# Performance work log

Hardware: AMD Instinct MI355X
Metric: run time of the kernel (lower is better)

Reference implementation:

```python
import jax, jax.numpy as jnp
import numpy as np


def _conv1x1(x, w, b=None):
    # x: [B, Cin, N, S], w: [Cout, Cin], 1x1 Conv2d
    y = jnp.einsum('oc,bcns->bons', w, x)
    if b is not None:
        y = y + b[None, :, None, None]
    return y


def setup_inputs() -> dict:
    key = jax.random.key(0)
    ks = jax.random.split(key, 16)
    B, Cin, N, K = 4, 128, 16384, 16
    MID, OUT, SHARE, PT = 64, 128, 8, 10
    s = 0.05
    inp = {
        'sm_feats': jax.random.normal(ks[0], (B, Cin, N, K), jnp.float32),
        'sm_ppfs': jax.random.normal(ks[1], (B, PT, N, K), jnp.float32),
        'conv0_w': jax.random.normal(ks[2], (OUT, Cin), jnp.float32) * s,
        'conv0_b': jax.random.normal(ks[3], (OUT,), jnp.float32) * s,
        'conv1_w': jax.random.normal(ks[4], (MID, OUT), jnp.float32) * s,
        'conv1_b': jax.random.normal(ks[5], (MID,), jnp.float32) * s,
        'conv2_w': jax.random.normal(ks[6], (MID, OUT), jnp.float32) * s,
        'conv2_b': jax.random.normal(ks[7], (MID,), jnp.float32) * s,
        'conv3_w': jax.random.normal(ks[8], (MID, OUT), jnp.float32) * s,
        'conv3_b': jax.random.normal(ks[9], (MID,), jnp.float32) * s,
        'convw1_w': jax.random.normal(ks[10], (MID // SHARE, MID * K), jnp.float32) * s,
        'convw2_w': jax.random.normal(ks[11], (K * MID // SHARE, MID // SHARE), jnp.float32) * s,
        'convw2_b': jax.random.normal(ks[12], (K * MID // SHARE,), jnp.float32) * s,
        'convout_w': jax.random.normal(ks[13], (OUT, MID), jnp.float32) * s,
        'convout_b': jax.random.normal(ks[14], (OUT,), jnp.float32) * s,
        'pt1_w': jax.random.normal(ks[15], (MID, PT), jnp.float32) * s,
        'pt2_w': jax.random.normal(jax.random.fold_in(key, 99), (MID, MID), jnp.float32) * s,
    }
    return inp


def reference(sm_feats, sm_ppfs, conv0_w, conv0_b, conv1_w, conv1_b, conv2_w, conv2_b,
              conv3_w, conv3_b, convw1_w, convw2_w, convw2_b, convout_w, convout_b,
              pt1_w, pt2_w):
    xn = jax.nn.relu(_conv1x1(sm_feats, conv0_w, conv0_b))  # [B, OUT, N, K]
    x = xn[..., :1]                                          # center point feature
    identity = x
    x1 = _conv1x1(x, conv1_w, conv1_b)       # [B, MID, N, 1]
    x2 = _conv1x1(xn, conv2_w, conv2_b)      # [B, MID, N, K]
    x3 = _conv1x1(xn, conv3_w, conv3_b)      # [B, MID, N, K]
    ptf = _conv1x1(jax.nn.relu(_conv1x1(sm_ppfs, pt1_w)), pt2_w)  # [B, MID, N, K]
    x3 = x3 + ptf
    xfs = x1 - x2 + ptf                      # [B, MID, N, K]
    B, MID, N, K = xfs.shape
    share = MID // convw1_w.shape[0]
    xfs = jnp.transpose(xfs, (0, 1, 3, 2)).reshape(B, MID * K, 1, N)
    h = jax.nn.relu(_conv1x1(xfs, convw1_w))            # [B, MID//share, 1, N]
    w = _conv1x1(h, convw2_w, convw2_b)                  # [B, K*MID//share, 1, N]
    w = jax.nn.softmax(w.reshape(B, MID // share, K, N), axis=2)
    w = jnp.transpose(w, (0, 1, 3, 2))                   # [B, MID//share, N, K]
    w = jnp.tile(w, (1, share, 1, 1))                    # [B, MID, N, K]
    out = jax.nn.relu(jnp.sum(w * x3, axis=3, keepdims=True))  # [B, MID, N, 1]
    out = (_conv1x1(out, convout_w, convout_b) + identity).squeeze(3)  # [B, OUT, N]
    return out
```

## Files before the change

### kernel.cpp

```cpp
#include <hip/hip_runtime.h>
#include <hip/hip_bf16.h>


typedef __attribute__((ext_vector_type(8))) short bf16x8;
typedef __attribute__((ext_vector_type(4))) float f32x4;
typedef __attribute__((ext_vector_type(4))) unsigned short us4;

#define MFMA(a, b, c) __builtin_amdgcn_mfma_f32_16x16x32_bf16((a), (b), (c), 0, 0, 0)

#define OFF_F    0
#define OFF_X2   0
#define OFF_PTF  17408
#define OFF_XN   34816
#define OFF_X3   34816
#define OFF_XFS  52224
#define OFF_P    69632
#define OFF_WS   69632
#define OFF_HP   73984
#define OFF_HB   76032
#define OFF_OM   76288
#define OFF_X1   77824
#define OFF_XC   78912
#define SMEM_BYTES 81088

#define WS_W0  0
#define WS_W1  16384
#define WS_W2  24576
#define WS_W3  32768
#define WS_P1  40960
#define WS_P2  43008
#define WS_CW1 47104
#define WS_WO  63488
#define WS_TOTAL 71680

__device__ __forceinline__ unsigned short f2b(float f) {
    union { __hip_bfloat16 h; unsigned short u; } v;
    v.h = __float2bfloat16(f);
    return v.u;
}
__device__ __forceinline__ float b2f(unsigned short u) {
    union { unsigned u; float f; } v;
    v.u = ((unsigned)u) << 16;
    return v.f;
}
__device__ __forceinline__ us4 pk4(float a, float b, float c, float d) {
    us4 r; r[0] = f2b(a); r[1] = f2b(b); r[2] = f2b(c); r[3] = f2b(d); return r;
}
__device__ __forceinline__ bf16x8 ldb(const unsigned short* p) {
    return *(const bf16x8*)p;
}

__global__ __launch_bounds__(512, 1)
void convert_weights(const float* __restrict__ w0, const float* __restrict__ w1,
                     const float* __restrict__ w2, const float* __restrict__ w3,
                     const float* __restrict__ p1, const float* __restrict__ p2,
                     const float* __restrict__ cw1, const float* __restrict__ wo,
                     unsigned short* __restrict__ ws) {
    int i = blockIdx.x * 512 + threadIdx.x;
    if (i >= WS_TOTAL) return;
    float v;
    if (i < 16384)      v = w0[i];
    else if (i < 24576) v = w1[i - 16384];
    else if (i < 32768) v = w2[i - 24576];
    else if (i < 40960) v = w3[i - 32768];
    else if (i < 43008) { int r = i - 40960, row = r >> 5, k = r & 31;
                          v = (k < 10) ? p1[row * 10 + k] : 0.f; }
    else if (i < 47104) v = p2[i - 43008];
    else if (i < 63488) { int r = i - 47104, j = r >> 10, kc = r & 1023;
                          v = (j < 8) ? cw1[j * 1024 + (kc & 63) * 16 + (kc >> 6)] : 0.f; }
    else                v = wo[i - 63488];
    ws[i] = f2b(v);
}

__global__ __launch_bounds__(512, 4)
void fused_model_kernel(const float* __restrict__ feats, const float* __restrict__ ppfs,
                        const unsigned short* __restrict__ wsb,
                        const float* __restrict__ b0, const float* __restrict__ b1,
                        const float* __restrict__ b2, const float* __restrict__ b3,
                        const float* __restrict__ cw2, const float* __restrict__ cb2,
                        const float* __restrict__ bo, float* __restrict__ out) {
    extern __shared__ char smem[];
    const int tid = threadIdx.x;
    const int W = tid >> 6;
    const int lane = tid & 63;
    const int kk = lane & 15;
    const int g = lane >> 4;
    const int bid = blockIdx.x;
    const int b = bid >> 11;
    const int n0 = (bid & 2047) * 8;

    {
        const int kq = tid & 3, ci = tid >> 2;
        const int cisw = (ci * 2) ^ (kq << 4);
        #pragma unroll
        for (int pos = 0; pos < 8; ++pos) {
            f32x4 v = *(const f32x4*)(feats + (((size_t)b * 128 + ci) * 16384 + (n0 + pos)) * 16 + kq * 4);
            char* base = smem + OFF_F + pos * 4352 + cisw;
            *(unsigned short*)(base + (kq * 4 + 0) * 272) = f2b(v[0]);
            *(unsigned short*)(base + (kq * 4 + 1) * 272) = f2b(v[1]);
            *(unsigned short*)(base + (kq * 4 + 2) * 272) = f2b(v[2]);
            *(unsigned short*)(base + (kq * 4 + 3) * 272) = f2b(v[3]);
        }
        if (tid < 320) {
            int pos = tid / 40, r = tid % 40, p = r >> 2, kq2 = r & 3;
            f32x4 v = *(const f32x4*)(ppfs + (((size_t)b * 10 + p) * 16384 + (n0 + pos)) * 16 + kq2 * 4);
            char* base = smem + OFF_P + pos * 1024 + p * 2;
            *(unsigned short*)(base + (kq2 * 4 + 0) * 64) = f2b(v[0]);
            *(unsigned short*)(base + (kq2 * 4 + 1) * 64) = f2b(v[1]);
            *(unsigned short*)(base + (kq2 * 4 + 2) * 64) = f2b(v[2]);
            *(unsigned short*)(base + (kq2 * 4 + 3) * 64) = f2b(v[3]);
        } else {
            for (int z = tid - 320; z < 1408; z += 192) {
                int pos = z / 176, rr = z % 176, ks = rr / 11, dw = rr % 11;
                *(unsigned*)(smem + OFF_P + pos * 1024 + ks * 64 + 20 + dw * 4) = 0u;
            }
        }
    }
    __syncthreads();

    {
        bf16x8 a0[4];
        #pragma unroll
        for (int kt = 0; kt < 4; ++kt) a0[kt] = ldb(wsb + WS_W0 + (16 * W + kk) * 128 + kt * 32 + 8 * g);
        f32x4 bv = *(const f32x4*)(b0 + 16 * W + 4 * g);
        const int fsw = ((kk >> 2) & 3) << 4;
        #pragma unroll
        for (int pos = 0; pos < 8; ++pos) {
            f32x4 acc = {0.f, 0.f, 0.f, 0.f};
            #pragma unroll
            for (int kt = 0; kt < 4; ++kt) {
                bf16x8 bf = *(const bf16x8*)(smem + OFF_F + pos * 4352 + kk * 272 + ((kt * 64 + 16 * g) ^ fsw));
                acc = MFMA(a0[kt], bf, acc);
            }
            us4 xw = pk4(fmaxf(acc[0] + bv[0], 0.f), fmaxf(acc[1] + bv[1], 0.f),
                         fmaxf(acc[2] + bv[2], 0.f), fmaxf(acc[3] + bv[3], 0.f));
            *(us4*)(smem + OFF_XN + pos * 4352 + kk * 272 + (16 * W + 4 * g) * 2) = xw;
            if (kk == 0) *(us4*)(smem + OFF_XC + pos * 272 + (16 * W + 4 * g) * 2) = xw;
        }
    }
    __syncthreads();

    if (W < 4) {
        bf16x8 a1[4], a2[4][2];
        #pragma unroll
        for (int mt = 0; mt < 4; ++mt) {
            a1[mt] = ldb(wsb + WS_P1 + (16 * mt + kk) * 32 + 8 * g);
            a2[mt][0] = ldb(wsb + WS_P2 + (16 * mt + kk) * 64 + 8 * g);
            a2[mt][1] = ldb(wsb + WS_P2 + (16 * mt + kk) * 64 + 32 + 8 * g);
        }
        const int sel = g >> 1;
        const int sa = kk + 16 * ((2 * g) & 3);
        const int sb = kk + 16 * ((2 * g + 1) & 3);
        #pragma unroll
        for (int pp = 0; pp < 2; ++pp) {
            const int pos = 2 * W + pp;
            bf16x8 bp = *(const bf16x8*)(smem + OFF_P + pos * 1024 + kk * 64 + 16 * g);
            int pkd[4][2];
            #pragma unroll
            for (int mt = 0; mt < 4; ++mt) {
                f32x4 hv = {0.f, 0.f, 0.f, 0.f};
                hv = MFMA(a1[mt], bp, hv);
                us4 t = pk4(fmaxf(hv[0], 0.f), fmaxf(hv[1], 0.f),
                            fmaxf(hv[2], 0.f), fmaxf(hv[3], 0.f));
                pkd[mt][0] = ((int*)&t)[0];
                pkd[mt][1] = ((int*)&t)[1];
            }
            union { int d[4]; bf16x8 v; } bh0, bh1;
            bh0.d[0] = sel ? __shfl(pkd[1][0], sa, 64) : __shfl(pkd[0][0], sa, 64);
            bh0.d[1] = sel ? __shfl(pkd[1][1], sa, 64) : __shfl(pkd[0][1], sa, 64);
            bh0.d[2] = sel ? __shfl(pkd[1][0], sb, 64) : __shfl(pkd[0][0], sb, 64);
            bh0.d[3] = sel ? __shfl(pkd[1][1], sb, 64) : __shfl(pkd[0][1], sb, 64);
            bh1.d[0] = sel ? __shfl(pkd[3][0], sa, 64) : __shfl(pkd[2][0], sa, 64);
            bh1.d[1] = sel ? __shfl(pkd[3][1], sa, 64) : __shfl(pkd[2][1], sa, 64);
            bh1.d[2] = sel ? __shfl(pkd[3][0], sb, 64) : __shfl(pkd[2][0], sb, 64);
            bh1.d[3] = sel ? __shfl(pkd[3][1], sb, 64) : __shfl(pkd[2][1], sb, 64);
            #pragma unroll
            for (int mt = 0; mt < 4; ++mt) {
                f32x4 acc = {0.f, 0.f, 0.f, 0.f};
                acc = MFMA(a2[mt][0], bh0.v, acc);
                acc = MFMA(a2[mt][1], bh1.v, acc);
                *(us4*)(smem + OFF_PTF + pos * 2176 + kk * 136 + (16 * mt + 4 * g) * 2) =
                    pk4(acc[0], acc[1], acc[2], acc[3]);
            }
        }
    } else {
        const int mt = W - 4;
        bf16x8 aw2[4], aw1[4];
        #pragma unroll
        for (int kt = 0; kt < 4; ++kt) {
            aw2[kt] = ldb(wsb + WS_W2 + (16 * mt + kk) * 128 + kt * 32 + 8 * g);
            aw1[kt] = ldb(wsb + WS_W1 + (16 * mt + kk) * 128 + kt * 32 + 8 * g);
        }
        f32x4 b2v = *(const f32x4*)(b2 + 16 * mt + 4 * g);
        #pragma unroll
        for (int pos = 0; pos < 8; ++pos) {
            f32x4 acc = {0.f, 0.f, 0.f, 0.f};
            #pragma unroll
            for (int kt = 0; kt < 4; ++kt) {
                bf16x8 bf = *(const bf16x8*)(smem + OFF_XN + pos * 4352 + kk * 272 + (kt * 64 + 16 * g));
                acc = MFMA(aw2[kt], bf, acc);
            }
            *(us4*)(smem + OFF_X2 + pos * 2176 + kk * 136 + (16 * mt + 4 * g) * 2) =
                pk4(acc[0] + b2v[0], acc[1] + b2v[1], acc[2] + b2v[2], acc[3] + b2v[3]);
        }
        f32x4 a1c = {0.f, 0.f, 0.f, 0.f};
        #pragma unroll
        for (int kt = 0; kt < 4; ++kt) {
            bf16x8 bf = *(const bf16x8*)(smem + OFF_XC + (kk & 7) * 272 + (kt * 64 + 16 * g));
            a1c = MFMA(aw1[kt], bf, a1c);
        }
        if (kk < 8) {
            f32x4 b1v = *(const f32x4*)(b1 + 16 * mt + 4 * g);
            *(us4*)(smem + OFF_X1 + kk * 136 + (16 * mt + 4 * g) * 2) =
                pk4(a1c[0] + b1v[0], a1c[1] + b1v[1], a1c[2] + b1v[2], a1c[3] + b1v[3]);
        }
    }
    __syncthreads();

    f32x4 acc3[4];
    {
        const int mt = W & 3, ph = W >> 2;
        bf16x8 aw3[4];
        #pragma unroll
        for (int kt = 0; kt < 4; ++kt)
            aw3[kt] = ldb(wsb + WS_W3 + (16 * mt + kk) * 128 + kt * 32 + 8 * g);
        #pragma unroll
        for (int pp = 0; pp < 4; ++pp) {
            const int pos = ph * 4 + pp;
            f32x4 acc = {0.f, 0.f, 0.f, 0.f};
            #pragma unroll
            for (int kt = 0; kt < 4; ++kt) {
                bf16x8 bf = *(const bf16x8*)(smem + OFF_XN + pos * 4352 + kk * 272 + (kt * 64 + 16 * g));
                acc = MFMA(aw3[kt], bf, acc);
            }
            acc3[pp] = acc;
        }
    }
    __syncthreads();

    {
        const int mt = W & 3, ph = W >> 2;
        f32x4 b3v = *(const f32x4*)(b3 + 16 * mt + 4 * g);
        const int rot = (32 * mt + 8 * g + 16 * kk) & 127;
        #pragma unroll
        for (int pp = 0; pp < 4; ++pp) {
            const int pos = ph * 4 + pp;
            us4 ptfv = *(const us4*)(smem + OFF_PTF + pos * 2176 + kk * 136 + (16 * mt + 4 * g) * 2);
            us4 x2v  = *(const us4*)(smem + OFF_X2  + pos * 2176 + kk * 136 + (16 * mt + 4 * g) * 2);
            us4 x1v  = *(const us4*)(smem + OFF_X1  + pos * 136 + (16 * mt + 4 * g) * 2);
            float pf0 = b2f(ptfv[0]), pf1 = b2f(ptfv[1]), pf2 = b2f(ptfv[2]), pf3 = b2f(ptfv[3]);
            *(us4*)(smem + OFF_X3 + pos * 2176 + kk * 136 + (16 * mt + 4 * g) * 2) =
                pk4(acc3[pp][0] + b3v[0] + pf0, acc3[pp][1] + b3v[1] + pf1,
                    acc3[pp][2] + b3v[2] + pf2, acc3[pp][3] + b3v[3] + pf3);
            *(us4*)(smem + OFF_XFS + pos * 2080 + kk * 128 + rot) =
                pk4(b2f(x1v[0]) - b2f(x2v[0]) + pf0, b2f(x1v[1]) - b2f(x2v[1]) + pf1,
                    b2f(x1v[2]) - b2f(x2v[2]) + pf2, b2f(x1v[3]) - b2f(x2v[3]) + pf3);
        }
    }
    __syncthreads();

    {
        bf16x8 acw[4];
        #pragma unroll
        for (int kt = 0; kt < 4; ++kt)
            acw[kt] = ldb(wsb + WS_CW1 + kk * 1024 + W * 128 + kt * 32 + 8 * g);
        const char* xb = smem + OFF_XFS + (kk & 7) * 2080;
        f32x4 acc = {0.f, 0.f, 0.f, 0.f};
        #pragma unroll
        for (int kt = 0; kt < 4; ++kt) {
            const int k = 2 * W + (kt >> 1);
            const int byt = (64 * (kt & 1) + 16 * g + 16 * k) & 127;
            bf16x8 bf = *(const bf16x8*)(xb + k * 128 + byt);
            acc = MFMA(acw[kt], bf, acc);
        }
        if (kk < 8 && g < 2) {
            #pragma unroll
            for (int r = 0; r < 4; ++r)
                *(float*)(smem + OFF_HP + W * 256 + ((4 * g + r) * 8 + kk) * 4) = acc[r];
        }
    }
    __syncthreads();
    if (tid < 64) {
        float s = 0.f;
        #pragma unroll
        for (int w = 0; w < 8; ++w) s += *(const float*)(smem + OFF_HP + w * 256 + tid * 4);
        *(float*)(smem + OFF_HB + tid * 4) = fmaxf(s, 0.f);
    }
    __syncthreads();

    {
        #pragma unroll
        for (int pp = 0; pp < 2; ++pp) {
            const int item = tid + 512 * pp;
            const int pos = item >> 7, c = item & 127, k = c & 15, j2 = c >> 4;
            float wl = cb2[c];
            f32x4 w20 = *(const f32x4*)(cw2 + c * 8);
            f32x4 w21 = *(const f32x4*)(cw2 + c * 8 + 4);
            #pragma unroll
            for (int j = 0; j < 4; ++j) {
                wl += w20[j] * *(const float*)(smem + OFF_HB + (j * 8 + pos) * 4);
                wl += w21[j] * *(const float*)(smem + OFF_HB + ((j + 4) * 8 + pos) * 4);
            }
            float mx = wl;
            for (int off = 8; off; off >>= 1) mx = fmaxf(mx, __shfl_xor(mx, off, 16));
            float e = __expf(wl - mx);
            float ss = e;
            for (int off = 8; off; off >>= 1) ss += __shfl_xor(ss, off, 16);
            *(float*)(smem + OFF_WS + pos * 544 + j2 * 68 + k * 4) = e / ss;
        }
    }
    __syncthreads();

    {
        const int pos = W, m = lane, j2 = m & 7;
        const float* wsp = (const float*)(smem + OFF_WS + pos * 544 + j2 * 68);
        const char* x3b = smem + OFF_X3 + pos * 2176 + m * 2;
        float s = 0.f;
        #pragma unroll
        for (int k = 0; k < 16; ++k)
            s += wsp[k] * b2f(*(const unsigned short*)(x3b + k * 136));
        *(unsigned short*)(smem + OFF_OM + pos * 144 + m * 2) = f2b(fmaxf(s, 0.f));
    }
    __syncthreads();

    {
        f32x4 acc = {0.f, 0.f, 0.f, 0.f};
        #pragma unroll
        for (int kt = 0; kt < 2; ++kt) {
            bf16x8 bf = *(const bf16x8*)(smem + OFF_OM + (kk & 7) * 144 + (kt * 64 + 16 * g));
            acc = MFMA(ldb(wsb + WS_WO + (16 * W + kk) * 64 + kt * 32 + 8 * g), bf, acc);
        }
        if (kk < 8) {
            f32x4 bv = *(const f32x4*)(bo + 16 * W + 4 * g);
            #pragma unroll
            for (int r = 0; r < 4; ++r) {
                int o = 16 * W + 4 * g + r;
                out[((size_t)b * 128 + o) * 16384 + n0 + kk] =
                    acc[r] + bv[r] + b2f(*(const unsigned short*)(smem + OFF_XC + kk * 272 + o * 2));
            }
        }
    }
}

extern "C" void kernel_launch(void* const* d_in, const int* in_sizes, int n_in,
                              void* d_out, int out_size, void* d_ws, size_t ws_size,
                              hipStream_t stream) {
    (void)in_sizes; (void)n_in; (void)out_size; (void)ws_size;
    const float* feats = (const float*)d_in[0];
    const float* ppfs  = (const float*)d_in[1];
    const float* w0  = (const float*)d_in[2];
    const float* b0  = (const float*)d_in[3];
    const float* w1  = (const float*)d_in[4];
    const float* b1  = (const float*)d_in[5];
    const float* w2  = (const float*)d_in[6];
    const float* b2  = (const float*)d_in[7];
    const float* w3  = (const float*)d_in[8];
    const float* b3  = (const float*)d_in[9];
    const float* cw1 = (const float*)d_in[10];
    const float* cw2 = (const float*)d_in[11];
    const float* cb2 = (const float*)d_in[12];
    const float* wo  = (const float*)d_in[13];
    const float* bo  = (const float*)d_in[14];
    const float* p1  = (const float*)d_in[15];
    const float* p2  = (const float*)d_in[16];
    float* out = (float*)d_out;
    unsigned short* wsb = (unsigned short*)d_ws;

    convert_weights<<<dim3((WS_TOTAL + 511) / 512), dim3(512), 0, stream>>>(
        w0, w1, w2, w3, p1, p2, cw1, wo, wsb);

    (void)hipFuncSetAttribute(reinterpret_cast<const void*>(fused_model_kernel),
                              hipFuncAttributeMaxDynamicSharedMemorySize, SMEM_BYTES);
    fused_model_kernel<<<dim3(8192), dim3(512), SMEM_BYTES, stream>>>(
        feats, ppfs, wsb, b0, b1, b2, b3, cw2, cb2, bo, out);
}
```

Measured before the change: 318.5 us.

## Merge conv stages, cut barriers, preload weights, and atomically reduce hidden layer

Weight fragments for conv0, conv1, conv2 and conv3 are now loaded into registers at kernel start so they overlap with the input staging. The conv3 work is split across the two wave groups: the ptf waves compute conv3 for the first four positions plus conv1, and the conv2 waves reuse their loaded xn fragments for conv3 on the last four. This removes one stage and its barrier. The hidden-layer partial sums are reduced with shared-memory atomicAdd into a zeroed buffer instead of a partial array plus a serial reduction. The softmax and weighted-sum steps are fused per wave using a wave barrier and vectorised loads, which saves two more block barriers at the cost of LDS atomic contention and higher register pressure.

Measured after the change: 303.6 us. 4.7% less time.

```diff
diff --git a/kernel.cpp b/kernel.cpp
--- a/kernel.cpp
+++ b/kernel.cpp
@@ -16,8 +16,7 @@
 #define OFF_XFS  52224
 #define OFF_P    69632
 #define OFF_WS   69632
-#define OFF_HP   73984
-#define OFF_HB   76032
+#define OFF_HB   74752
 #define OFF_OM   76288
 #define OFF_X1   77824
 #define OFF_XC   78912
@@ -89,6 +88,22 @@
     const int b = bid >> 11;
     const int n0 = (bid & 2047) * 8;
 
+    bf16x8 a0[4], rA[4], rB[4];
+    {
+        const int mtr = (W & 3);
+        #pragma unroll
+        for (int kt = 0; kt < 4; ++kt) {
+            a0[kt] = ldb(wsb + WS_W0 + (16 * W + kk) * 128 + kt * 32 + 8 * g);
+            if (W < 4) {
+                rA[kt] = ldb(wsb + WS_W3 + (16 * mtr + kk) * 128 + kt * 32 + 8 * g);
+                rB[kt] = ldb(wsb + WS_W1 + (16 * mtr + kk) * 128 + kt * 32 + 8 * g);
+            } else {
+                rA[kt] = ldb(wsb + WS_W2 + (16 * mtr + kk) * 128 + kt * 32 + 8 * g);
+                rB[kt] = ldb(wsb + WS_W3 + (16 * mtr + kk) * 128 + kt * 32 + 8 * g);
+            }
+        }
+    }
+
     {
         const int kq = tid & 3, ci = tid >> 2;
         const int cisw = (ci * 2) ^ (kq << 4);
@@ -119,9 +134,6 @@
     __syncthreads();
 
     {
-        bf16x8 a0[4];
-        #pragma unroll
-        for (int kt = 0; kt < 4; ++kt) a0[kt] = ldb(wsb + WS_W0 + (16 * W + kk) * 128 + kt * 32 + 8 * g);
         f32x4 bv = *(const f32x4*)(b0 + 16 * W + 4 * g);
         const int fsw = ((kk >> 2) & 3) << 4;
         #pragma unroll
@@ -140,6 +152,7 @@
     }
     __syncthreads();
 
+    f32x4 acc3[4];
     if (W < 4) {
         bf16x8 a1[4], a2[4][2];
         #pragma unroll
@@ -183,57 +196,47 @@
                     pk4(acc[0], acc[1], acc[2], acc[3]);
             }
         }
+        #pragma unroll
+        for (int pp = 0; pp < 4; ++pp) {
+            f32x4 acc = {0.f, 0.f, 0.f, 0.f};
+            #pragma unroll
+            for (int kt = 0; kt < 4; ++kt) {
+                bf16x8 bf = *(const bf16x8*)(smem + OFF_XN + pp * 4352 + kk * 272 + (kt * 64 + 16 * g));
+                acc = MFMA(rA[kt], bf, acc);
+            }
+            acc3[pp] = acc;
+        }
+        f32x4 a1c = {0.f, 0.f, 0.f, 0.f};
+        #pragma unroll
+        for (int kt = 0; kt < 4; ++kt) {
+            bf16x8 bf = *(const bf16x8*)(smem + OFF_XC + (kk & 7) * 272 + (kt * 64 + 16 * g));
+            a1c = MFMA(rB[kt], bf, a1c);
+        }
+        if (kk < 8) {
+            f32x4 b1v = *(const f32x4*)(b1 + 16 * W + 4 * g);
+            *(us4*)(smem + OFF_X1 + kk * 136 + (16 * W + 4 * g) * 2) =
+                pk4(a1c[0] + b1v[0], a1c[1] + b1v[1], a1c[2] + b1v[2], a1c[3] + b1v[3]);
+        }
     } else {
         const int mt = W - 4;
-        bf16x8 aw2[4], aw1[4];
-        #pragma unroll
-        for (int kt = 0; kt < 4; ++kt) {
-            aw2[kt] = ldb(wsb + WS_W2 + (16 * mt + kk) * 128 + kt * 32 + 8 * g);
-            aw1[kt] = ldb(wsb + WS_W1 + (16 * mt + kk) * 128 + kt * 32 + 8 * g);
-        }
         f32x4 b2v = *(const f32x4*)(b2 + 16 * mt + 4 * g);
         #pragma unroll
         for (int pos = 0; pos < 8; ++pos) {
+            bf16x8 bx[4];
+            #pragma unroll
+            for (int kt = 0; kt < 4; ++kt)
+                bx[kt] = *(const bf16x8*)(smem + OFF_XN + pos * 4352 + kk * 272 + (kt * 64 + 16 * g));
             f32x4 acc = {0.f, 0.f, 0.f, 0.f};
             #pragma unroll
-            for (int kt = 0; kt < 4; ++kt) {
-                bf16x8 bf = *(const bf16x8*)(smem + OFF_XN + pos * 4352 + kk * 272 + (kt * 64 + 16 * g));
-                acc = MFMA(aw2[kt], bf, acc);
-            }
+            for (int kt = 0; kt < 4; ++kt) acc = MFMA(rA[kt], bx[kt], acc);
             *(us4*)(smem + OFF_X2 + pos * 2176 + kk * 136 + (16 * mt + 4 * g) * 2) =
                 pk4(acc[0] + b2v[0], acc[1] + b2v[1], acc[2] + b2v[2], acc[3] + b2v[3]);
-        }
-        f32x4 a1c = {0.f, 0.f, 0.f, 0.f};
-        #pragma unroll
-        for (int kt = 0; kt < 4; ++kt) {
-            bf16x8 bf = *(const bf16x8*)(smem + OFF_XC + (kk & 7) * 272 + (kt * 64 + 16 * g));
-            a1c = MFMA(aw1[kt], bf, a1c);
-        }
-        if (kk < 8) {
-            f32x4 b1v = *(const f32x4*)(b1 + 16 * mt + 4 * g);
-            *(us4*)(smem + OFF_X1 + kk * 136 + (16 * mt + 4 * g) * 2) =
-                pk4(a1c[0] + b1v[0], a1c[1] + b1v[1], a1c[2] + b1v[2], a1c[3] + b1v[3]);
-        }
-    }
-    __syncthreads();
-
-    f32x4 acc3[4];
-    {
-        const int mt = W & 3, ph = W >> 2;
-        bf16x8 aw3[4];
-        #pragma unroll
-        for (int kt = 0; kt < 4; ++kt)
-            aw3[kt] = ldb(wsb + WS_W3 + (16 * mt + kk) * 128 + kt * 32 + 8 * g);
-        #pragma unroll
-        for (int pp = 0; pp < 4; ++pp) {
-            const int pos = ph * 4 + pp;
-            f32x4 acc = {0.f, 0.f, 0.f, 0.f};
-            #pragma unroll
-            for (int kt = 0; kt < 4; ++kt) {
-                bf16x8 bf = *(const bf16x8*)(smem + OFF_XN + pos * 4352 + kk * 272 + (kt * 64 + 16 * g));
-                acc = MFMA(aw3[kt], bf, acc);
-            }
-            acc3[pp] = acc;
+            if (pos >= 4) {
+                f32x4 c = {0.f, 0.f, 0.f, 0.f};
+                #pragma unroll
+                for (int kt = 0; kt < 4; ++kt) c = MFMA(rB[kt], bx[kt], c);
+                acc3[pos - 4] = c;
+            }
         }
     }
     __syncthreads();
@@ -256,6 +259,7 @@
                 pk4(b2f(x1v[0]) - b2f(x2v[0]) + pf0, b2f(x1v[1]) - b2f(x2v[1]) + pf1,
                     b2f(x1v[2]) - b2f(x2v[2]) + pf2, b2f(x1v[3]) - b2f(x2v[3]) + pf3);
         }
+        if (tid < 64) *(float*)(smem + OFF_HB + tid * 4) = 0.f;
     }
     __syncthreads();
 
@@ -276,50 +280,54 @@
         if (kk < 8 && g < 2) {
             #pragma unroll
             for (int r = 0; r < 4; ++r)
-                *(float*)(smem + OFF_HP + W * 256 + ((4 * g + r) * 8 + kk) * 4) = acc[r];
-        }
-    }
-    __syncthreads();
-    if (tid < 64) {
-        float s = 0.f;
-        #pragma unroll
-        for (int w = 0; w < 8; ++w) s += *(const float*)(smem + OFF_HP + w * 256 + tid * 4);
-        *(float*)(smem + OFF_HB + tid * 4) = fmaxf(s, 0.f);
-    }
-    __syncthreads();
-
-    {
-        #pragma unroll
-        for (int pp = 0; pp < 2; ++pp) {
-            const int item = tid + 512 * pp;
-            const int pos = item >> 7, c = item & 127, k = c & 15, j2 = c >> 4;
+                atomicAdd((float*)(smem + OFF_HB + kk * 32 + (4 * g + r) * 4), acc[r]);
+        }
+    }
+    __syncthreads();
+
+    {
+        const int pos = W;
+        f32x4 h0 = *(const f32x4*)(smem + OFF_HB + pos * 32);
+        f32x4 h1 = *(const f32x4*)(smem + OFF_HB + pos * 32 + 16);
+        #pragma unroll
+        for (int r = 0; r < 4; ++r) { h0[r] = fmaxf(h0[r], 0.f); h1[r] = fmaxf(h1[r], 0.f); }
+        #pragma unroll
+        for (int it = 0; it < 2; ++it) {
+            const int c = it * 64 + lane;
             float wl = cb2[c];
             f32x4 w20 = *(const f32x4*)(cw2 + c * 8);
             f32x4 w21 = *(const f32x4*)(cw2 + c * 8 + 4);
             #pragma unroll
             for (int j = 0; j < 4; ++j) {
-                wl += w20[j] * *(const float*)(smem + OFF_HB + (j * 8 + pos) * 4);
-                wl += w21[j] * *(const float*)(smem + OFF_HB + ((j + 4) * 8 + pos) * 4);
+                wl += w20[j] * h0[j];
+                wl += w21[j] * h1[j];
             }
             float mx = wl;
             for (int off = 8; off; off >>= 1) mx = fmaxf(mx, __shfl_xor(mx, off, 16));
             float e = __expf(wl - mx);
             float ss = e;
             for (int off = 8; off; off >>= 1) ss += __shfl_xor(ss, off, 16);
-            *(float*)(smem + OFF_WS + pos * 544 + j2 * 68 + k * 4) = e / ss;
-        }
-    }
-    __syncthreads();
-
-    {
-        const int pos = W, m = lane, j2 = m & 7;
-        const float* wsp = (const float*)(smem + OFF_WS + pos * 544 + j2 * 68);
-        const char* x3b = smem + OFF_X3 + pos * 2176 + m * 2;
+            *(float*)(smem + OFF_WS + pos * 640 + (4 * it + g) * 80 + kk * 4) = e / ss;
+        }
+        __builtin_amdgcn_wave_barrier();
+        __builtin_amdgcn_sched_barrier(0);
+
+        const char* wsp = smem + OFF_WS + pos * 640 + (lane & 7) * 80;
+        f32x4 wv0 = *(const f32x4*)(wsp);
+        f32x4 wv1 = *(const f32x4*)(wsp + 16);
+        f32x4 wv2 = *(const f32x4*)(wsp + 32);
+        f32x4 wv3 = *(const f32x4*)(wsp + 48);
+        const char* x3b = smem + OFF_X3 + pos * 2176 + lane * 2;
         float s = 0.f;
         #pragma unroll
-        for (int k = 0; k < 16; ++k)
-            s += wsp[k] * b2f(*(const unsigned short*)(x3b + k * 136));
-        *(unsigned short*)(smem + OFF_OM + pos * 144 + m * 2) = f2b(fmaxf(s, 0.f));
+        for (int k = 0; k < 4; ++k) s += wv0[k] * b2f(*(const unsigned short*)(x3b + k * 136));
+        #pragma unroll
+        for (int k = 0; k < 4; ++k) s += wv1[k] * b2f(*(const unsigned short*)(x3b + (k + 4) * 136));
+        #pragma unroll
+        for (int k = 0; k < 4; ++k) s += wv2[k] * b2f(*(const unsigned short*)(x3b + (k + 8) * 136));
+        #pragma unroll
+        for (int k = 0; k < 4; ++k) s += wv3[k] * b2f(*(const unsigned short*)(x3b + (k + 12) * 136));
+        *(unsigned short*)(smem + OFF_OM + pos * 144 + lane * 2) = f2b(fmaxf(s, 0.f));
     }
     __syncthreads();
 
@@ -332,11 +340,11 @@
         }
         if (kk < 8) {
             f32x4 bv = *(const f32x4*)(bo + 16 * W + 4 * g);
+            us4 xcv = *(const us4*)(smem + OFF_XC + kk * 272 + (16 * W + 4 * g) * 2);
             #pragma unroll
             for (int r = 0; r < 4; ++r) {
                 int o = 16 * W + 4 * g + r;
-                out[((size_t)b * 128 + o) * 16384 + n0 + kk] =
-                    acc[r] + bv[r] + b2f(*(const unsigned short*)(smem + OFF_XC + kk * 272 + o * 2));
+                out[((size_t)b * 128 + o) * 16384 + n0 + kk] = acc[r] + bv[r] + b2f(xcv[r]);
             }
         }
     }
```
